# Performance work log

Measured on AMD Instinct MI355X. Metric: run time of the kernel, lower is better.

Reference implementation:

```python
import jax, jax.numpy as jnp
import numpy as np

DIM = 128
GRID = 8
RED = 16  # LCBAM channel-attention reduction
B, L = 16, 4096


def setup_inputs() -> dict:
    key = jax.random.key(0)
    ks = jax.random.split(key, 8)
    scale = 1.0 / (np.sqrt(DIM) * np.sqrt(GRID))
    return {
        "x": jax.random.normal(ks[0], (B, L, DIM), jnp.float32),
        "n1_g": jnp.ones((DIM,), jnp.float32),
        "n1_b": jnp.zeros((DIM,), jnp.float32),
        "fk1_c": jax.random.normal(ks[1], (2, DIM, DIM, GRID), jnp.float32) * scale,
        "fk1_b": jnp.zeros((DIM,), jnp.float32),
        "n2_g": jnp.ones((DIM,), jnp.float32),
        "n2_b": jnp.zeros((DIM,), jnp.float32),
        "fk2_c": jax.random.normal(ks[2], (2, DIM, DIM, GRID), jnp.float32) * scale,
        "fk2_b": jnp.zeros((DIM,), jnp.float32),
        "w1": jax.random.normal(ks[3], (DIM // RED, DIM), jnp.float32) * 0.05,  # channel-MLP reduce
        "w2": jax.random.normal(ks[4], (DIM, DIM // RED), jnp.float32) * 0.05,  # channel-MLP expand
        "conv_w": jax.random.normal(ks[5], (1, 2, 7, 7), jnp.float32) * 0.05,   # spatial-attn 7x7 conv
    }


def _layernorm(x, g, b, eps=1e-5):
    m = jnp.mean(x, axis=-1, keepdims=True)
    v = jnp.var(x, axis=-1, keepdims=True)
    return (x - m) * jax.lax.rsqrt(v + eps) * g + b


def _fkan(x, coeffs, bias):
    # x: (B,L,I); coeffs: (2,O,I,G)
    k = jnp.arange(1, GRID + 1, dtype=x.dtype)          # (G,)
    ang = x[..., None] * k                               # (B,L,I,G)
    y = jnp.einsum("blig,oig->blo", jnp.cos(ang), coeffs[0])
    y = y + jnp.einsum("blig,oig->blo", jnp.sin(ang), coeffs[1])
    return y + bias


def reference(x, n1_g, n1_b, fk1_c, fk1_b, n2_g, n2_b, fk2_c, fk2_b, w1, w2, conv_w):
    residual = x
    out = _fkan(_layernorm(x, n1_g, n1_b), fk1_c, fk1_b)
    out = jax.nn.relu(out)
    out = _fkan(_layernorm(out, n2_g, n2_b), fk2_c, fk2_b)
    b, l, c = out.shape
    x4 = out.reshape(b, c, 1, l)  # faithful to torch .view (raw reshape, not transpose)
    # LCBAM channel attention: avg+max pool -> shared MLP -> sigmoid
    avg = jnp.mean(x4, axis=(2, 3))   # (B,C)
    mx = jnp.max(x4, axis=(2, 3))     # (B,C)
    mlp = lambda v: jax.nn.relu(v @ w1.T) @ w2.T
    ca = jax.nn.sigmoid(mlp(avg) + mlp(mx))[:, :, None, None]
    x4 = x4 * ca
    # LCBAM spatial attention: channel mean/max -> 7x7 conv -> sigmoid
    s_in = jnp.concatenate([jnp.mean(x4, axis=1, keepdims=True),
                            jnp.max(x4, axis=1, keepdims=True)], axis=1)  # (B,2,1,L)
    sa = jax.lax.conv_general_dilated(s_in, conv_w, (1, 1), ((3, 3), (3, 3)))
    x4 = x4 * jax.nn.sigmoid(sa)
    out = x4.reshape(b, l, c)
    return residual + out
```

## Files before the change

### kernel.cpp

```cpp
#include <hip/hip_runtime.h>
#include <math.h>

typedef unsigned short ushort_t;
typedef unsigned int uint_t;
typedef _Float16 half_t;

#define DIMC 128
#define NB 16
#define NL 4096

using f32x4 = __attribute__((ext_vector_type(4))) float;
using bf16x8 = __attribute__((ext_vector_type(8))) short;
using half4 = __attribute__((ext_vector_type(4))) half_t;

__device__ __forceinline__ ushort_t bf16rne(float f) {
  uint_t b = __float_as_uint(f);
  b += 0x7fffu + ((b >> 16) & 1u);
  return (ushort_t)(b >> 16);
}

__device__ __forceinline__ uint_t pkbf(float lo, float hi) {
  union { __bf16 h[2]; uint_t u; } u;
  u.h[0] = (__bf16)lo;
  u.h[1] = (__bf16)hi;
  return u.u;
}

__device__ __forceinline__ float bf2f(ushort_t u) {
  return __uint_as_float(((uint_t)u) << 16);
}

__global__ __launch_bounds__(256) void prep_coef_k(const float* __restrict__ fk1,
                                                   const float* __restrict__ fk2,
                                                   ushort_t* __restrict__ coefT) {
  int idx = blockIdx.x * 256 + threadIdx.x;
  int layer = idx >> 15;
  int rem = idx & 32767;
  int ci = rem >> 11;
  int n = (rem >> 8) & 7;
  int s = (rem >> 6) & 3;
  int l = rem & 63;
  int o = n * 16 + (l & 15);
  int kbase = ci * 128 + s * 32 + (l >> 4) * 8;
  const float* src = layer ? fk2 : fk1;
  uint_t p[4];
#pragma unroll
  for (int jj = 0; jj < 4; ++jj) {
    int k0 = kbase + jj * 2;
    int t0 = k0 & 1, g0 = (k0 >> 1) & 7, i0 = k0 >> 4;
    int k1 = k0 + 1;
    int t1 = k1 & 1, g1 = (k1 >> 1) & 7, i1 = k1 >> 4;
    ushort_t a = bf16rne(src[((t0 * DIMC + o) * DIMC + i0) * 8 + g0]);
    ushort_t b = bf16rne(src[((t1 * DIMC + o) * DIMC + i1) * 8 + g1]);
    p[jj] = (uint_t)a | ((uint_t)b << 16);
  }
  uint4 w;
  w.x = p[0]; w.y = p[1]; w.z = p[2]; w.w = p[3];
  *(uint4*)&coefT[idx * 8] = w;
}

constexpr int SXH = 132;

__global__ __launch_bounds__(256, 2) void fkan_main_k(
    const float* __restrict__ x,
    const float* __restrict__ n1g, const float* __restrict__ n1b,
    const float* __restrict__ fk1b,
    const float* __restrict__ n2g, const float* __restrict__ n2b,
    const float* __restrict__ fk2b,
    const ushort_t* __restrict__ coefT,
    ushort_t* __restrict__ out2,
    float* __restrict__ chanSum, float* __restrict__ chanMax) {

  __shared__ half_t xln[128 * SXH];
  __shared__ uint4 feat[4][2][2][64];

  const int tid = threadIdx.x;
  const int bid = blockIdx.x;
  const int lane = tid & 63;
  const int wid = tid >> 6;
  const int rowBase = wid * 32;
  const size_t tileBase = (size_t)bid * 128 * DIMC;

  {
    const float4* src = (const float4*)(x + tileBase + (size_t)rowBase * DIMC);
#pragma unroll
    for (int j = 0; j < 16; ++j) {
      int idx = j * 64 + lane;
      float4 v = src[idx];
      half4 h;
      h.x = (half_t)v.x; h.y = (half_t)v.y; h.z = (half_t)v.z; h.w = (half_t)v.w;
      *(half4*)&xln[(rowBase + (idx >> 5)) * SXH + (idx & 31) * 4] = h;
    }
  }

  auto layernorm = [&](const float* gg, const float* bb) {
    float g0 = gg[lane], g1 = gg[lane + 64];
    float be0 = bb[lane], be1 = bb[lane + 64];
#pragma unroll
    for (int j = 0; j < 32; ++j) {
      int t = rowBase + j;
      float v0 = (float)xln[t * SXH + lane], v1 = (float)xln[t * SXH + 64 + lane];
      float s = v0 + v1, q = v0 * v0 + v1 * v1;
#pragma unroll
      for (int m = 1; m < 64; m <<= 1) {
        s += __shfl_xor(s, m, 64);
        q += __shfl_xor(q, m, 64);
      }
      float mean = s * (1.0f / DIMC);
      float var = q * (1.0f / DIMC) - mean * mean;
      float rr = rsqrtf(var + 1e-5f);
      xln[t * SXH + lane] = (half_t)((v0 - mean) * rr * g0 + be0);
      xln[t * SXH + 64 + lane] = (half_t)((v1 - mean) * rr * g1 + be1);
    }
  };

  layernorm(n1g, n1b);

  const int tl = lane & 31;
  const int chOff = lane >> 5;
  const int mmw = tl >> 4;
  const int l0 = (tl & 15) + (chOff << 5);
  const half_t* xch = &xln[(rowBase + tl) * SXH + chOff];

  auto chain_gen = [&](int chunk, int ns, int nbuf) {
    float a = (float)xch[chunk * 8 + ns * 2];
    float s1, c1;
    __sincosf(a, &s1, &c1);
    uint_t q0 = pkbf(c1, s1);
    float ck = c1, sk = s1, cn, sn;
    cn = ck * c1 - sk * s1; sn = sk * c1 + ck * s1; ck = cn; sk = sn;
    uint_t q1 = pkbf(ck, sk);
    cn = ck * c1 - sk * s1; sn = sk * c1 + ck * s1; ck = cn; sk = sn;
    uint_t q2 = pkbf(ck, sk);
    cn = ck * c1 - sk * s1; sn = sk * c1 + ck * s1; ck = cn; sk = sn;
    uint_t q3 = pkbf(ck, sk);
    cn = ck * c1 - sk * s1; sn = sk * c1 + ck * s1; ck = cn; sk = sn;
    uint_t q4 = pkbf(ck, sk);
    cn = ck * c1 - sk * s1; sn = sk * c1 + ck * s1; ck = cn; sk = sn;
    uint_t q5 = pkbf(ck, sk);
    cn = ck * c1 - sk * s1; sn = sk * c1 + ck * s1; ck = cn; sk = sn;
    uint_t q6 = pkbf(ck, sk);
    cn = ck * c1 - sk * s1; sn = sk * c1 + ck * s1; ck = cn; sk = sn;
    uint_t q7 = pkbf(ck, sk);
    uint4 w0; w0.x = q0; w0.y = q1; w0.z = q2; w0.w = q3;
    uint4 w1; w1.x = q4; w1.y = q5; w1.z = q6; w1.w = q7;
    feat[wid][nbuf][mmw][l0] = w0;
    feat[wid][nbuf][mmw][l0 + 16] = w1;
  };

  f32x4 acc[8][2];

  auto ldB = [&](const ushort_t* cbase, int ci, int s, bf16x8 (&bf)[8]) {
#pragma unroll
    for (int nn = 0; nn < 8; ++nn)
      bf[nn] = *(const bf16x8*)(cbase +
          (size_t)((((ci * 8 + nn) * 4 + s) << 6) + lane) * 8);
  };

  auto mfma16 = [&](bf16x8 a0, bf16x8 a1, bf16x8 (&bf)[8]) {
    __builtin_amdgcn_s_setprio(1);
#pragma unroll
    for (int nn = 0; nn < 8; ++nn) {
      acc[nn][0] = __builtin_amdgcn_mfma_f32_16x16x32_bf16(a0, bf[nn],
                                                           acc[nn][0], 0, 0, 0);
      acc[nn][1] = __builtin_amdgcn_mfma_f32_16x16x32_bf16(a1, bf[nn],
                                                           acc[nn][1], 0, 0, 0);
    }
    __builtin_amdgcn_s_setprio(0);
  };

  auto run_layer = [&](const ushort_t* cbase) {
#pragma unroll
    for (int nn = 0; nn < 8; ++nn)
#pragma unroll
      for (int mm = 0; mm < 2; ++mm) acc[nn][mm] = (f32x4)(0.f);
    chain_gen(0, 0, 0);
#pragma unroll 1
    for (int ci = 0; ci < 16; ++ci) {
#pragma unroll
      for (int j = 0; j < 4; ++j) {
        bf16x8 bf[8];
        ldB(cbase, ci, j, bf);
        const int cb = j & 1;
        bf16x8 a0 = *(const bf16x8*)&feat[wid][cb][0][lane];
        bf16x8 a1 = *(const bf16x8*)&feat[wid][cb][1][lane];
        const int nstep = ci * 4 + j + 1;
        chain_gen((nstep >> 2) & 15, nstep & 3, nstep & 1);
        mfma16(a0, a1, bf);
      }
    }
  };

  run_layer(coefT);

#pragma unroll
  for (int nn = 0; nn < 8; ++nn) {
    int o = nn * 16 + (lane & 15);
    float bia = fk1b[o];
#pragma unroll
    for (int mm = 0; mm < 2; ++mm) {
      int trow = rowBase + mm * 16 + (lane >> 4) * 4;
#pragma unroll
      for (int r = 0; r < 4; ++r)
        xln[(trow + r) * SXH + o] = (half_t)fmaxf(acc[nn][mm][r] + bia, 0.f);
    }
  }

  layernorm(n2g, n2b);

  run_layer(coefT + 262144);

  float ls = 0.f, lm = -INFINITY;
#pragma unroll
  for (int nn = 0; nn < 8; ++nn) {
    int o = nn * 16 + (lane & 15);
    float bia = fk2b[o];
#pragma unroll
    for (int mm = 0; mm < 2; ++mm) {
      int trow = rowBase + mm * 16 + (lane >> 4) * 4;
#pragma unroll
      for (int r = 0; r < 4; ++r) {
        float v = acc[nn][mm][r] + bia;
        out2[tileBase + (size_t)(trow + r) * DIMC + o] = bf16rne(v);
        ls += v;
        lm = fmaxf(lm, v);
      }
    }
  }
#pragma unroll
  for (int m = 1; m < 64; m <<= 1) {
    ls += __shfl_xor(ls, m, 64);
    lm = fmaxf(lm, __shfl_xor(lm, m, 64));
  }
  if (lane == 0) {
    chanSum[bid * 4 + wid] = ls;
    chanMax[bid * 4 + wid] = lm;
  }
}

__global__ __launch_bounds__(128) void tail_k(
    const float* __restrict__ x, const ushort_t* __restrict__ out2,
    const float* __restrict__ chanSum, const float* __restrict__ chanMax,
    const float* __restrict__ w1, const float* __restrict__ w2,
    const float* __restrict__ convw, float* __restrict__ dout) {
  int b = blockIdx.x >> 5;
  int t = blockIdx.x & 31;
  int c = threadIdx.x;
  __shared__ float avs[DIMC], mxs[DIMC], hh[16], cas[DIMC];
  __shared__ float sM[134], sX[134];

  avs[c] = chanSum[b * DIMC + c] * (1.0f / NL);
  mxs[c] = chanMax[b * DIMC + c];
  __syncthreads();
  if (c < 16) {
    const float* v = (c < 8) ? avs : mxs;
    float a = 0.f;
    for (int i = 0; i < DIMC; ++i) a += v[i] * w1[(c & 7) * DIMC + i];
    hh[c] = fmaxf(a, 0.f);
  }
  __syncthreads();
  {
    float z = 0.f;
#pragma unroll
    for (int r = 0; r < 8; ++r) z += (hh[r] + hh[8 + r]) * w2[c * 8 + r];
    cas[c] = 1.0f / (1.0f + expf(-z));
  }
  __syncthreads();

  const ushort_t* o2b = out2 + (size_t)b * NL * DIMC;
  float s = 0.f, m = -INFINITY;
#pragma unroll 4
  for (int c4 = 0; c4 < 128; ++c4) {
    float v = bf2f(o2b[(size_t)(c4 * 32 + t) * DIMC + c]) * cas[c4];
    s += v;
    m = fmaxf(m, v);
  }
  sM[c + 3] = s * (1.0f / DIMC);
  sX[c + 3] = m;
  if (c < 6) {
    bool left = c < 3;
    int tp = left ? t - 1 : t + 1;
    int cc = left ? 125 + c : c - 3;
    int di = left ? c : 131 + (c - 3);
    float ss = 0.f, mm2 = -INFINITY;
    if (tp >= 0 && tp < 32) {
#pragma unroll 4
      for (int c4 = 0; c4 < 128; ++c4) {
        float v = bf2f(o2b[(size_t)(c4 * 32 + tp) * DIMC + cc]) * cas[c4];
        ss += v;
        mm2 = fmaxf(mm2, v);
      }
      sM[di] = ss * (1.0f / DIMC);
      sX[di] = mm2;
    } else {
      sM[di] = 0.f;
      sX[di] = 0.f;
    }
  }
  __syncthreads();

  float sa = 0.f;
#pragma unroll
  for (int d = 0; d < 7; ++d)
    sa += convw[21 + d] * sM[c + d] + convw[70 + d] * sX[c + d];
  float sig = 1.0f / (1.0f + expf(-sa));

  const float* xb = x + (size_t)b * NL * DIMC;
  float* db = dout + (size_t)b * NL * DIMC;
#pragma unroll 2
  for (int c4 = 0; c4 < 128; ++c4) {
    size_t idx = (size_t)(c4 * 32 + t) * DIMC + c;
    db[idx] = xb[idx] + bf2f(o2b[idx]) * cas[c4] * sig;
  }
}

extern "C" void kernel_launch(void* const* d_in, const int* in_sizes, int n_in,
                              void* d_out, int out_size, void* d_ws, size_t ws_size,
                              hipStream_t stream) {
  const float* x = (const float*)d_in[0];
  const float* n1g = (const float*)d_in[1];
  const float* n1b = (const float*)d_in[2];
  const float* fk1c = (const float*)d_in[3];
  const float* fk1b = (const float*)d_in[4];
  const float* n2g = (const float*)d_in[5];
  const float* n2b = (const float*)d_in[6];
  const float* fk2c = (const float*)d_in[7];
  const float* fk2b = (const float*)d_in[8];
  const float* w1 = (const float*)d_in[9];
  const float* w2 = (const float*)d_in[10];
  const float* convw = (const float*)d_in[11];

  ushort_t* out2 = (ushort_t*)d_ws;
  ushort_t* coefT = out2 + 8388608;
  float* chanSum = (float*)(coefT + 524288);
  float* chanMax = chanSum + 2048;
  float* dout = (float*)d_out;

  prep_coef_k<<<256, 256, 0, stream>>>(fk1c, fk2c, coefT);
  fkan_main_k<<<512, 256, 0, stream>>>(x, n1g, n1b, fk1b, n2g, n2b,
                                       fk2b, coefT, out2, chanSum, chanMax);
  tail_k<<<NB * 32, 128, 0, stream>>>(x, out2, chanSum, chanMax, w1, w2, convw, dout);
}
```

Before: 153.1 us.

## Retile FKAN GEMM to 2x2 wave grid with shared features and B prefetch

Switches each block's 128x128 output tile from four 32-row-per-wave strips to a 2x2 wave grid of 64x64 sub-tiles. Sine/cosine feature generation is now shared across the block through LDS, so each wave loads half as many coefficient fragments per step. Coefficient loads are double-buffered in registers one step ahead. The cost is a block-wide barrier every K step plus extra syncs around the layernorm stages, and the channel sum/max reduction is regrouped through shared memory.

```diff
diff --git a/kernel.cpp b/kernel.cpp
--- a/kernel.cpp
+++ b/kernel.cpp
@@ -28,6 +28,12 @@
 
 __device__ __forceinline__ float bf2f(ushort_t u) {
   return __uint_as_float(((uint_t)u) << 16);
+}
+
+__device__ __forceinline__ void lds_barrier() {
+  asm volatile("s_waitcnt lgkmcnt(0)" ::: "memory");
+  __builtin_amdgcn_s_barrier();
+  asm volatile("" ::: "memory");
 }
 
 __global__ __launch_bounds__(256) void prep_coef_k(const float* __restrict__ fk1,
@@ -72,33 +78,36 @@
     float* __restrict__ chanSum, float* __restrict__ chanMax) {
 
   __shared__ half_t xln[128 * SXH];
-  __shared__ uint4 feat[4][2][2][64];
+  __shared__ uint4 feat[2][8][64];
+  __shared__ float sredS[4][2], sredM[4][2];
 
   const int tid = threadIdx.x;
   const int bid = blockIdx.x;
   const int lane = tid & 63;
   const int wid = tid >> 6;
-  const int rowBase = wid * 32;
+  const int mw = wid >> 1;
+  const int nw = wid & 1;
   const size_t tileBase = (size_t)bid * 128 * DIMC;
 
   {
-    const float4* src = (const float4*)(x + tileBase + (size_t)rowBase * DIMC);
+    const float4* src = (const float4*)(x + tileBase);
 #pragma unroll
     for (int j = 0; j < 16; ++j) {
-      int idx = j * 64 + lane;
+      int idx = j * 256 + tid;
       float4 v = src[idx];
       half4 h;
       h.x = (half_t)v.x; h.y = (half_t)v.y; h.z = (half_t)v.z; h.w = (half_t)v.w;
-      *(half4*)&xln[(rowBase + (idx >> 5)) * SXH + (idx & 31) * 4] = h;
-    }
-  }
+      *(half4*)&xln[(idx >> 5) * SXH + (idx & 31) * 4] = h;
+    }
+  }
+  __syncthreads();
 
   auto layernorm = [&](const float* gg, const float* bb) {
     float g0 = gg[lane], g1 = gg[lane + 64];
     float be0 = bb[lane], be1 = bb[lane + 64];
 #pragma unroll
     for (int j = 0; j < 32; ++j) {
-      int t = rowBase + j;
+      int t = wid * 32 + j;
       float v0 = (float)xln[t * SXH + lane], v1 = (float)xln[t * SXH + 64 + lane];
       float s = v0 + v1, q = v0 * v0 + v1 * v1;
 #pragma unroll
@@ -115,15 +124,16 @@
   };
 
   layernorm(n1g, n1b);
-
-  const int tl = lane & 31;
-  const int chOff = lane >> 5;
-  const int mmw = tl >> 4;
-  const int l0 = (tl & 15) + (chOff << 5);
-  const half_t* xch = &xln[(rowBase + tl) * SXH + chOff];
-
-  auto chain_gen = [&](int chunk, int ns, int nbuf) {
-    float a = (float)xch[chunk * 8 + ns * 2];
+  __syncthreads();
+
+  const int ft = tid & 127;
+  const int fco = tid >> 7;
+  const int fmt = ft >> 4;
+  const int fslot = (ft & 15) + (fco << 5);
+  const half_t* fx = &xln[ft * SXH];
+
+  auto chain_gen = [&](int step, int nbuf) {
+    float a = (float)fx[((step >> 2) & 15) * 8 + (step & 3) * 2 + fco];
     float s1, c1;
     __sincosf(a, &s1, &c1);
     uint_t q0 = pkbf(c1, s1);
@@ -144,97 +154,112 @@
     uint_t q7 = pkbf(ck, sk);
     uint4 w0; w0.x = q0; w0.y = q1; w0.z = q2; w0.w = q3;
     uint4 w1; w1.x = q4; w1.y = q5; w1.z = q6; w1.w = q7;
-    feat[wid][nbuf][mmw][l0] = w0;
-    feat[wid][nbuf][mmw][l0 + 16] = w1;
-  };
-
-  f32x4 acc[8][2];
-
-  auto ldB = [&](const ushort_t* cbase, int ci, int s, bf16x8 (&bf)[8]) {
-#pragma unroll
-    for (int nn = 0; nn < 8; ++nn)
-      bf[nn] = *(const bf16x8*)(cbase +
-          (size_t)((((ci * 8 + nn) * 4 + s) << 6) + lane) * 8);
-  };
-
-  auto mfma16 = [&](bf16x8 a0, bf16x8 a1, bf16x8 (&bf)[8]) {
+    feat[nbuf][fmt][fslot] = w0;
+    feat[nbuf][fmt][fslot + 16] = w1;
+  };
+
+  f32x4 acc[4][4];
+
+  auto ldB = [&](const ushort_t* cbase, int step, bf16x8 (&bf)[4]) {
+    int ci = (step >> 2) & 15, s = step & 3;
+#pragma unroll
+    for (int nt = 0; nt < 4; ++nt)
+      bf[nt] = *(const bf16x8*)(cbase +
+          (size_t)((((ci * 8 + nw * 4 + nt) * 4 + s) << 6) + lane) * 8);
+  };
+
+  auto do_step = [&](const ushort_t* cbase, int step, int par,
+                     bf16x8 (&bfCur)[4], bf16x8 (&bfNext)[4]) {
+    bf16x8 af[4];
+#pragma unroll
+    for (int k = 0; k < 4; ++k)
+      af[k] = *(const bf16x8*)&feat[par][mw * 4 + k][lane];
+    ldB(cbase, step + 1, bfNext);
+    chain_gen(step + 1, par ^ 1);
     __builtin_amdgcn_s_setprio(1);
 #pragma unroll
-    for (int nn = 0; nn < 8; ++nn) {
-      acc[nn][0] = __builtin_amdgcn_mfma_f32_16x16x32_bf16(a0, bf[nn],
-                                                           acc[nn][0], 0, 0, 0);
-      acc[nn][1] = __builtin_amdgcn_mfma_f32_16x16x32_bf16(a1, bf[nn],
-                                                           acc[nn][1], 0, 0, 0);
-    }
+    for (int nt = 0; nt < 4; ++nt)
+#pragma unroll
+      for (int mt = 0; mt < 4; ++mt)
+        acc[nt][mt] = __builtin_amdgcn_mfma_f32_16x16x32_bf16(
+            af[mt], bfCur[nt], acc[nt][mt], 0, 0, 0);
     __builtin_amdgcn_s_setprio(0);
+    lds_barrier();
   };
 
   auto run_layer = [&](const ushort_t* cbase) {
 #pragma unroll
-    for (int nn = 0; nn < 8; ++nn)
-#pragma unroll
-      for (int mm = 0; mm < 2; ++mm) acc[nn][mm] = (f32x4)(0.f);
-    chain_gen(0, 0, 0);
+    for (int nt = 0; nt < 4; ++nt)
+#pragma unroll
+      for (int mt = 0; mt < 4; ++mt) acc[nt][mt] = (f32x4)(0.f);
+    bf16x8 bfA[4], bfB[4];
+    ldB(cbase, 0, bfA);
+    chain_gen(0, 0);
+    lds_barrier();
 #pragma unroll 1
-    for (int ci = 0; ci < 16; ++ci) {
-#pragma unroll
-      for (int j = 0; j < 4; ++j) {
-        bf16x8 bf[8];
-        ldB(cbase, ci, j, bf);
-        const int cb = j & 1;
-        bf16x8 a0 = *(const bf16x8*)&feat[wid][cb][0][lane];
-        bf16x8 a1 = *(const bf16x8*)&feat[wid][cb][1][lane];
-        const int nstep = ci * 4 + j + 1;
-        chain_gen((nstep >> 2) & 15, nstep & 3, nstep & 1);
-        mfma16(a0, a1, bf);
+    for (int it = 0; it < 32; ++it) {
+      do_step(cbase, it * 2, 0, bfA, bfB);
+      do_step(cbase, it * 2 + 1, 1, bfB, bfA);
+    }
+  };
+
+  run_layer(coefT);
+  __syncthreads();
+
+#pragma unroll
+  for (int nt = 0; nt < 4; ++nt) {
+    int o = nw * 64 + nt * 16 + (lane & 15);
+    float bia = fk1b[o];
+#pragma unroll
+    for (int mt = 0; mt < 4; ++mt) {
+      int trow = mw * 64 + mt * 16 + (lane >> 4) * 4;
+#pragma unroll
+      for (int r = 0; r < 4; ++r)
+        xln[(trow + r) * SXH + o] = (half_t)fmaxf(acc[nt][mt][r] + bia, 0.f);
+    }
+  }
+  __syncthreads();
+
+  layernorm(n2g, n2b);
+  __syncthreads();
+
+  run_layer(coefT + 262144);
+  __syncthreads();
+
+  float ls0 = 0.f, ls1 = 0.f, lm0 = -INFINITY, lm1 = -INFINITY;
+#pragma unroll
+  for (int nt = 0; nt < 4; ++nt) {
+    int o = nw * 64 + nt * 16 + (lane & 15);
+    float bia = fk2b[o];
+#pragma unroll
+    for (int mt = 0; mt < 4; ++mt) {
+      int trow = mw * 64 + mt * 16 + (lane >> 4) * 4;
+#pragma unroll
+      for (int r = 0; r < 4; ++r) {
+        float v = acc[nt][mt][r] + bia;
+        out2[tileBase + (size_t)(trow + r) * DIMC + o] = bf16rne(v);
+        if (mt < 2) { ls0 += v; lm0 = fmaxf(lm0, v); }
+        else        { ls1 += v; lm1 = fmaxf(lm1, v); }
       }
     }
-  };
-
-  run_layer(coefT);
-
-#pragma unroll
-  for (int nn = 0; nn < 8; ++nn) {
-    int o = nn * 16 + (lane & 15);
-    float bia = fk1b[o];
-#pragma unroll
-    for (int mm = 0; mm < 2; ++mm) {
-      int trow = rowBase + mm * 16 + (lane >> 4) * 4;
-#pragma unroll
-      for (int r = 0; r < 4; ++r)
-        xln[(trow + r) * SXH + o] = (half_t)fmaxf(acc[nn][mm][r] + bia, 0.f);
-    }
-  }
-
-  layernorm(n2g, n2b);
-
-  run_layer(coefT + 262144);
-
-  float ls = 0.f, lm = -INFINITY;
-#pragma unroll
-  for (int nn = 0; nn < 8; ++nn) {
-    int o = nn * 16 + (lane & 15);
-    float bia = fk2b[o];
-#pragma unroll
-    for (int mm = 0; mm < 2; ++mm) {
-      int trow = rowBase + mm * 16 + (lane >> 4) * 4;
-#pragma unroll
-      for (int r = 0; r < 4; ++r) {
-        float v = acc[nn][mm][r] + bia;
-        out2[tileBase + (size_t)(trow + r) * DIMC + o] = bf16rne(v);
-        ls += v;
-        lm = fmaxf(lm, v);
-      }
-    }
   }
 #pragma unroll
   for (int m = 1; m < 64; m <<= 1) {
-    ls += __shfl_xor(ls, m, 64);
-    lm = fmaxf(lm, __shfl_xor(lm, m, 64));
+    ls0 += __shfl_xor(ls0, m, 64);
+    ls1 += __shfl_xor(ls1, m, 64);
+    lm0 = fmaxf(lm0, __shfl_xor(lm0, m, 64));
+    lm1 = fmaxf(lm1, __shfl_xor(lm1, m, 64));
   }
   if (lane == 0) {
-    chanSum[bid * 4 + wid] = ls;
-    chanMax[bid * 4 + wid] = lm;
+    sredS[2 * mw + 0][nw] = ls0;
+    sredS[2 * mw + 1][nw] = ls1;
+    sredM[2 * mw + 0][nw] = lm0;
+    sredM[2 * mw + 1][nw] = lm1;
+  }
+  __syncthreads();
+  if (tid < 4) {
+    chanSum[bid * 4 + tid] = sredS[tid][0] + sredS[tid][1];
+    chanMax[bid * 4 + tid] = fmaxf(sredM[tid][0], sredM[tid][1]);
   }
 }
 
```

After: 157.9 us. 1.03x slower.
